# Optimization experiments

Measured on AMD Instinct MI355X. Metric: run time of the kernel, lower is better.

## Reference

```python
import jax, jax.numpy as jnp
import numpy as np

EPS_DIAG = 1e-4
EPS_SOFT = 1e-5
SCALE_DIV = 100000.0


def _cov2cor(x):
    # x: [N, C, d, d]; scale rows and cols by 1/sqrt(|diag|) (== D^-1 @ x @ D^-1)
    dia = jnp.abs(jnp.diagonal(x, axis1=-2, axis2=-1))          # [N, C, d]
    inv = 1.0 / jnp.sqrt(jnp.maximum(dia, EPS_DIAG))
    cor = x * inv[..., :, None] * inv[..., None, :]
    return jnp.clip(cor, -1.0, 1.0)


def _soft_pd_max(x):
    # x: [N, C, d, d]
    x = x - jnp.max(x, axis=(2, 3), keepdims=True)
    e = jnp.exp(x)
    dia = jnp.sum(e, axis=-1)                                    # [N, C, d]
    dia = jnp.maximum(dia, jnp.sum(dia, axis=2, keepdims=True) / SCALE_DIV)
    dia = jnp.maximum(dia, EPS_SOFT)
    inv = 1.0 / jnp.sqrt(dia)
    return e * inv[..., :, None] * inv[..., None, :]


def setup_inputs() -> dict:
    key = jax.random.key(0)
    k0, k1, k2, k3 = jax.random.split(key, 4)
    N, C, d = 64, 64, 64
    inputs = jax.random.normal(k0, (N, C, d, d), dtype=jnp.float32)
    # NonNeg uniform [0, 2/C] init for queries/keys
    w_queries = jax.random.uniform(k1, (C, C), dtype=jnp.float32, minval=0.0, maxval=2.0 / C)
    w_keys = jax.random.uniform(k2, (C, C), dtype=jnp.float32, minval=0.0, maxval=2.0 / C)
    # values: |N(0, 1/sqrt(C))| column-L1-normalized
    wv = jnp.abs(jax.random.normal(k3, (C, C), dtype=jnp.float32) / jnp.sqrt(jnp.float32(C)))
    w_values = wv / jnp.sum(wv, axis=0)
    return {"inputs": inputs, "w_queries": w_queries, "w_keys": w_keys, "w_values": w_values}


def reference(inputs, w_queries, w_keys, w_values):
    cor = _cov2cor(inputs)                                       # [N, C, d, d]
    X = jnp.transpose(cor, (0, 2, 3, 1))                         # [N, d, d, C]
    XWQ = jnp.matmul(X, w_queries)                               # [N, d, d, C]
    XWK = jnp.matmul(X, w_keys)
    XWV = jnp.matmul(X, w_values)
    XWQt = jnp.transpose(XWQ, (0, 3, 1, 2))                      # [N, C, d, d]
    XWKt = jnp.transpose(XWK, (0, 3, 2, 1))                      # [N, C, d, d] (transposed within dxd)
    XWKT = jnp.transpose(XWK, (0, 3, 1, 2))
    A_pre = jnp.matmul(jnp.matmul(XWKt, XWQt), XWKT)             # [N, C, d, d]
    A = _soft_pd_max(A_pre)
    V = jnp.transpose(XWV, (0, 3, 1, 2))                         # [N, C, d, d]
    AXA = jnp.matmul(jnp.matmul(A, V), jnp.transpose(A, (0, 1, 3, 2)))
    return inputs + AXA
```

## Files before the change

kernel.cpp:

```cpp
#include <hip/hip_runtime.h>

#define PITCH 72
#define ZP 136

typedef __attribute__((ext_vector_type(8))) short short8v;
typedef __attribute__((ext_vector_type(4))) short short4v;
typedef __attribute__((ext_vector_type(4))) float f32x4;

__device__ __forceinline__ short f2bf(float v) {
    unsigned u = __builtin_bit_cast(unsigned, v);
    unsigned r = (u + 0x7FFFu + ((u >> 16) & 1u)) >> 16;
    return (short)r;
}
__device__ __forceinline__ float bf2f(short s) {
    unsigned u = ((unsigned)(unsigned short)s) << 16;
    return __builtin_bit_cast(float, u);
}

#define MFMA(a, b, c) __builtin_amdgcn_mfma_f32_16x16x32_bf16(a, b, c, 0, 0, 0)

__device__ __forceinline__ short8v ldfrag(const short* p, int rowtile, int kc, int l) {
    return *(const short8v*)&p[(rowtile * 16 + (l & 15)) * PITCH + kc * 32 + (l >> 4) * 8];
}
__device__ __forceinline__ short8v gfrag(const short* __restrict__ p, int rowtile, int kc, int l) {
    return *(const short8v*)&p[(rowtile * 16 + (l & 15)) * 64 + kc * 32 + (l >> 4) * 8];
}

__device__ __forceinline__ void p1(const short* xh, const short* yh,
                                   int w, int l, f32x4 (&acc)[4]) {
#pragma unroll
    for (int ct = 0; ct < 4; ++ct) acc[ct] = (f32x4){0.f, 0.f, 0.f, 0.f};
#pragma unroll
    for (int kc = 0; kc < 2; ++kc) {
        short8v aH = ldfrag(xh, w, kc, l);
#pragma unroll
        for (int ct = 0; ct < 4; ++ct)
            acc[ct] = MFMA(aH, ldfrag(yh, ct, kc, l), acc[ct]);
    }
}

__device__ __forceinline__ void p1_g(const short* __restrict__ xg, const short* yh,
                                     int w, int l, f32x4 (&acc)[4]) {
#pragma unroll
    for (int ct = 0; ct < 4; ++ct) acc[ct] = (f32x4){0.f, 0.f, 0.f, 0.f};
#pragma unroll
    for (int kc = 0; kc < 2; ++kc) {
        short8v aH = gfrag(xg, w, kc, l);
#pragma unroll
        for (int ct = 0; ct < 4; ++ct)
            acc[ct] = MFMA(aH, ldfrag(yh, ct, kc, l), acc[ct]);
    }
}

__device__ __forceinline__ void p2v_g(const short* __restrict__ xg,
                                      const short* yh, const short* yl,
                                      int w, int l, f32x4 (&acc)[4]) {
#pragma unroll
    for (int ct = 0; ct < 4; ++ct) acc[ct] = (f32x4){0.f, 0.f, 0.f, 0.f};
#pragma unroll
    for (int kc = 0; kc < 2; ++kc) {
        short8v aH = gfrag(xg, w, kc, l);
#pragma unroll
        for (int ct = 0; ct < 4; ++ct) {
            acc[ct] = MFMA(aH, ldfrag(yh, ct, kc, l), acc[ct]);
            acc[ct] = MFMA(aH, ldfrag(yl, ct, kc, l), acc[ct]);
        }
    }
}

__device__ __forceinline__ void p2a(const short* xh, const short* xl,
                                    const short* yh,
                                    int w, int l, f32x4 (&acc)[4]) {
#pragma unroll
    for (int ct = 0; ct < 4; ++ct) acc[ct] = (f32x4){0.f, 0.f, 0.f, 0.f};
#pragma unroll
    for (int kc = 0; kc < 2; ++kc) {
        short8v aH = ldfrag(xh, w, kc, l);
        short8v aL = ldfrag(xl, w, kc, l);
#pragma unroll
        for (int ct = 0; ct < 4; ++ct) {
            short8v bH = ldfrag(yh, ct, kc, l);
            acc[ct] = MFMA(aH, bH, acc[ct]);
            acc[ct] = MFMA(aL, bH, acc[ct]);
        }
    }
}

__device__ __forceinline__ void pack1(const f32x4 (&acc)[4], short* zh, int w, int l) {
    int m0 = w * 16 + (l >> 4) * 4;
#pragma unroll
    for (int ct = 0; ct < 4; ++ct) {
        int n = ct * 16 + (l & 15);
        short4v h;
#pragma unroll
        for (int r = 0; r < 4; ++r) h[r] = f2bf(acc[ct][r]);
        *(short4v*)&zh[n * PITCH + m0] = h;
    }
}

__device__ __forceinline__ void idtrans_ip1(short* pa, int w, int l) {
    short8v a0 = ldfrag(pa, w, 0, l);
    short8v a1 = ldfrag(pa, w, 1, l);
    short8v I0, I1;
#pragma unroll
    for (int j = 0; j < 8; ++j) {
        int bit = 8 * (l >> 4) + j;
        I0[j] = (bit == (l & 15))      ? (short)0x3F80 : (short)0;
        I1[j] = (bit == (l & 15) + 16) ? (short)0x3F80 : (short)0;
    }
    __syncthreads();
    int m0 = w * 16 + (l >> 4) * 4;
    const f32x4 z4 = {0.f, 0.f, 0.f, 0.f};
#pragma unroll
    for (int s = 0; s < 4; ++s) {
        f32x4 d = MFMA((s >> 1) ? a1 : a0, (s & 1) ? I1 : I0, z4);
        short4v ha;
#pragma unroll
        for (int r = 0; r < 4; ++r) ha[r] = f2bf(d[r]);
        *(short4v*)&pa[(s * 16 + (l & 15)) * PITCH + m0] = ha;
    }
}

__device__ __forceinline__ void idtrans_ip2(short* pa, short* pb, int w, int l) {
    short8v a0 = ldfrag(pa, w, 0, l);
    short8v a1 = ldfrag(pa, w, 1, l);
    short8v b0 = ldfrag(pb, w, 0, l);
    short8v b1 = ldfrag(pb, w, 1, l);
    short8v I0, I1;
#pragma unroll
    for (int j = 0; j < 8; ++j) {
        int bit = 8 * (l >> 4) + j;
        I0[j] = (bit == (l & 15))      ? (short)0x3F80 : (short)0;
        I1[j] = (bit == (l & 15) + 16) ? (short)0x3F80 : (short)0;
    }
    __syncthreads();
    int m0 = w * 16 + (l >> 4) * 4;
    const f32x4 z4 = {0.f, 0.f, 0.f, 0.f};
#pragma unroll
    for (int s = 0; s < 4; ++s) {
        f32x4 d = MFMA((s >> 1) ? a1 : a0, (s & 1) ? I1 : I0, z4);
        f32x4 e = MFMA((s >> 1) ? b1 : b0, (s & 1) ? I1 : I0, z4);
        short4v ha, hb2;
#pragma unroll
        for (int r = 0; r < 4; ++r) { ha[r] = f2bf(d[r]); hb2[r] = f2bf(e[r]); }
        int drow = s * 16 + (l & 15);
        *(short4v*)&pa[drow * PITCH + m0] = ha;
        *(short4v*)&pb[drow * PITCH + m0] = hb2;
    }
}

__global__ __launch_bounds__(256) void k0_invdiag(const float* __restrict__ x,
                                                  float* __restrict__ invd) {
    int t = blockIdx.x * 256 + threadIdx.x;
    int nc = t >> 6, k = t & 63;
    float v = fabsf(x[(size_t)nc * 4096 + (size_t)k * 65]);
    invd[t] = rsqrtf(fmaxf(v, 1e-4f));
}

__global__ __launch_bounds__(256) void k0b_w3(const float* __restrict__ wq,
                                              const float* __restrict__ wk,
                                              const float* __restrict__ wv,
                                              short* __restrict__ w3h) {
    int idx = blockIdx.x * 256 + threadIdx.x;
    int co = idx >> 6, c = idx & 63;
    const float* w = (co < 64) ? wq : (co < 128) ? wk : wv;
    w3h[idx] = f2bf(w[c * 64 + (co & 63)]);
}

__global__ __launch_bounds__(256, 3) void k1_mix_mfma(
    const float* __restrict__ x, const float* __restrict__ invd,
    const short* __restrict__ w3h,
    short* __restrict__ Qh, short* __restrict__ Kh, short* __restrict__ Vh)
{
    __shared__ __align__(16) short smem[192 * ZP];
    short* ch0 = smem;
    short* ch1 = smem + 4608;

    const int b = blockIdx.x, n = b >> 5, ip = b & 31;
    const int t = threadIdx.x, l = t & 63, w = t >> 6;
    const size_t nbase = (size_t)n * 64;
    const int i0 = ip * 2;

#pragma unroll
    for (int rep = 0; rep < 8; ++rep) {
        int id = rep * 256 + t;
        int isel = id >> 10, rem = id & 1023;
        int c = rem >> 4, j4 = (rem & 15) * 4;
        int i = i0 + isel;
        float4 xv = *(const float4*)&x[((nbase + c) * 64 + i) * 64 + j4];
        float ii = invd[(nbase + c) * 64 + i];
        float4 jv = *(const float4*)&invd[(nbase + c) * 64 + j4];
        float vv[4] = {xv.x * ii * jv.x, xv.y * ii * jv.y,
                       xv.z * ii * jv.z, xv.w * ii * jv.w};
        short4v h;
#pragma unroll
        for (int r = 0; r < 4; ++r)
            h[r] = f2bf(fminf(1.0f, fmaxf(-1.0f, vv[r])));
        short* dst = isel ? ch1 : ch0;
        *(short4v*)&dst[c * PITCH + j4] = h;
    }
    __syncthreads();
    idtrans_ip2(ch0, ch1, w, l);
    __syncthreads();

    f32x4 a0[4][3], a1[4][3];
#pragma unroll
    for (int jt = 0; jt < 4; ++jt)
#pragma unroll
        for (int cc = 0; cc < 3; ++cc) {
            a0[jt][cc] = (f32x4){0.f, 0.f, 0.f, 0.f};
            a1[jt][cc] = (f32x4){0.f, 0.f, 0.f, 0.f};
        }
#pragma unroll
    for (int kc = 0; kc < 2; ++kc) {
        short8v f0[4], f1[4];
#pragma unroll
        for (int jt = 0; jt < 4; ++jt) {
            f0[jt] = ldfrag(ch0, jt, kc, l);
            f1[jt] = ldfrag(ch1, jt, kc, l);
        }
#pragma unroll
        for (int cc = 0; cc < 3; ++cc) {
            short8v bH = gfrag(w3h, w * 3 + cc, kc, l);
#pragma unroll
            for (int jt = 0; jt < 4; ++jt) {
                a0[jt][cc] = MFMA(f0[jt], bH, a0[jt][cc]);
                a1[jt][cc] = MFMA(f1[jt], bH, a1[jt][cc]);
            }
        }
    }
    __syncthreads();

    {
        int m0 = (l >> 4) * 4, nb = l & 15;
#pragma unroll
        for (int cc = 0; cc < 3; ++cc) {
            int nrow = (w * 3 + cc) * 16 + nb;
#pragma unroll
            for (int jt = 0; jt < 4; ++jt) {
                short4v h0, h1;
#pragma unroll
                for (int r = 0; r < 4; ++r) {
                    h0[r] = f2bf(a0[jt][cc][r]);
                    h1[r] = f2bf(a1[jt][cc][r]);
                }
                *(short4v*)&smem[nrow * ZP + jt * 16 + m0]      = h0;
                *(short4v*)&smem[nrow * ZP + 64 + jt * 16 + m0] = h1;
            }
        }
    }
    __syncthreads();

#pragma unroll
    for (int rep = 0; rep < 12; ++rep) {
        int id = rep * 256 + t;
        int row = id >> 4, c8 = (id & 15) * 8;
        short8v v = *(short8v*)&smem[row * ZP + c8];
        size_t off = (size_t)i0 * 64 + c8;
        if (rep < 4) {
            *(short8v*)&Qh[(nbase + row) * 4096 + off] = v;
        } else if (rep < 8) {
            *(short8v*)&Kh[(nbase + row - 64) * 4096 + off] = v;
        } else {
            *(short8v*)&Vh[(nbase + row - 128) * 4096 + off] = v;
        }
    }
}

__global__ __launch_bounds__(256, 5) void k2_attn_mfma(
    const float* __restrict__ x,
    const short* __restrict__ Qh, const short* __restrict__ Kh,
    const short* __restrict__ Vh,
    float* __restrict__ out)
{
    __shared__ __align__(16) short P[3][4608];
    __shared__ float part[4][64];
    __shared__ float invs[64];
    __shared__ float red[4];

    const int t = threadIdx.x, l = t & 63, w = t >> 6;
    const int nc = blockIdx.x;
    const size_t gbase = (size_t)nc * 4096;

    const short* qh = Qh + gbase;
    const short* kh = Kh + gbase;
    const short* vh = Vh + gbase;

#pragma unroll
    for (int rep = 0; rep < 4; ++rep) {
        int id = rep * 256 + t;
        int r = id >> 4, c4 = (id & 15) * 4;
        *(short4v*)&P[0][r * PITCH + c4] = *(const short4v*)&kh[r * 64 + c4];
    }
    __syncthreads();

    idtrans_ip1(P[0], w, l);
    __syncthreads();

    f32x4 acc[4];

    p1_g(qh, P[0], w, l, acc);
    pack1(acc, P[1], w, l);
    __syncthreads();

    p1(P[1], P[0], w, l, acc);

    float mx = -1e30f;
#pragma unroll
    for (int ct = 0; ct < 4; ++ct)
#pragma unroll
        for (int r = 0; r < 4; ++r) mx = fmaxf(mx, acc[ct][r]);
#pragma unroll
    for (int off = 1; off < 64; off <<= 1) mx = fmaxf(mx, __shfl_xor(mx, off));
    if (l == 0) red[w] = mx;
    __syncthreads();
    mx = fmaxf(fmaxf(red[0], red[1]), fmaxf(red[2], red[3]));

    float e[4][4];
    float cs[4];
#pragma unroll
    for (int ct = 0; ct < 4; ++ct) {
        float s = 0.f;
#pragma unroll
        for (int r = 0; r < 4; ++r) {
            float ev = __expf(acc[ct][r] - mx);
            e[ct][r] = ev;
            s += ev;
        }
        cs[ct] = s;
    }
#pragma unroll
    for (int ct = 0; ct < 4; ++ct) {
        cs[ct] += __shfl_xor(cs[ct], 16);
        cs[ct] += __shfl_xor(cs[ct], 32);
    }
    if (l < 16) {
#pragma unroll
        for (int ct = 0; ct < 4; ++ct) part[w][ct * 16 + l] = cs[ct];
    }
    __syncthreads();
    if (t < 64) {
        float dia = part[0][t] + part[1][t] + part[2][t] + part[3][t];
        float tot = dia;
#pragma unroll
        for (int off = 1; off < 64; off <<= 1) tot += __shfl_xor(tot, off);
        dia = fmaxf(dia, tot / 100000.0f);
        dia = fmaxf(dia, 1e-5f);
        invs[t] = rsqrtf(dia);
    }
    __syncthreads();

    {
        int m0 = w * 16 + (l >> 4) * 4;
        float ir[4] = {invs[m0], invs[m0 + 1], invs[m0 + 2], invs[m0 + 3]};
        int nb = l & 15;
#pragma unroll
        for (int ct = 0; ct < 4; ++ct) {
            float ic = invs[ct * 16 + nb];
            short4v h, lo;
#pragma unroll
            for (int r = 0; r < 4; ++r) {
                float v = e[ct][r] * ir[r] * ic;
                short hb = f2bf(v);
                h[r]  = hb;
                lo[r] = f2bf(v - bf2f(hb));
            }
            *(short4v*)&P[1][(ct * 16 + nb) * PITCH + m0] = h;
            *(short4v*)&P[0][(ct * 16 + nb) * PITCH + m0] = lo;
        }
    }
    __syncthreads();

    p2v_g(vh, P[1], P[0], w, l, acc);
    pack1(acc, P[2], w, l);
    __syncthreads();

    p2a(P[1], P[0], P[2], w, l, acc);
    __syncthreads();

    {
        float* ofs = (float*)&P[0][0];
        int m0 = w * 16 + (l >> 4) * 4;
        int nb = l & 15;
#pragma unroll
        for (int ct = 0; ct < 4; ++ct)
#pragma unroll
            for (int r = 0; r < 4; ++r)
                ofs[(m0 + r) * 68 + ct * 16 + nb] = acc[ct][r];
    }
    __syncthreads();
    {
        const float* ofs = (const float*)&P[0][0];
#pragma unroll
        for (int rep = 0; rep < 4; ++rep) {
            int id = rep * 256 + t;
            int row = id >> 4, c4 = (id & 15) * 4;
            float4 v  = *(const float4*)&ofs[row * 68 + c4];
            float4 xv = *(const float4*)&x[gbase + (size_t)row * 64 + c4];
            *(float4*)&out[gbase + (size_t)row * 64 + c4] =
                make_float4(xv.x + v.x, xv.y + v.y, xv.z + v.z, xv.w + v.w);
        }
    }
}

extern "C" void kernel_launch(void* const* d_in, const int* in_sizes, int n_in,
                              void* d_out, int out_size, void* d_ws, size_t ws_size,
                              hipStream_t stream) {
    const float* x  = (const float*)d_in[0];
    const float* wq = (const float*)d_in[1];
    const float* wk = (const float*)d_in[2];
    const float* wv = (const float*)d_in[3];
    float* out = (float*)d_out;

    char* wsb = (char*)d_ws;
    float* invd = (float*)wsb;
    short* w3h  = (short*)(wsb + (1 << 20));
    short* Qh   = (short*)(wsb + (2 << 20));
    short* Kh   = Qh + 16777216;
    short* Vh   = Kh + 16777216;

    k0_invdiag<<<1024, 256, 0, stream>>>(x, invd);
    k0b_w3<<<48, 256, 0, stream>>>(wq, wk, wv, w3h);
    k1_mix_mfma<<<2048, 256, 0, stream>>>(x, invd, w3h, Qh, Kh, Vh);
    k2_attn_mfma<<<4096, 256, 0, stream>>>(x, Qh, Kh, Vh, out);
}
```

Before: 92.88 us.

## Store Q/K/V in row-interleaved layout and merge prep kernels

Changes the intermediate Q/K/V layout from three separate [N,C,d,d] arrays to one interleaved buffer indexed by (n, i) rows of 192*64 elements, so k1 writes contiguous 1.5K-element chunks per i row with less LDS staging (smaller shared buffer, two half passes). k2 now reads its per-channel Q/K/V with a large stride of 12288 elements. The two small prep kernels are merged into one launch. This trades write coalescing and occupancy in k1 against strided 128-byte row reads in k2.

```diff
diff --git a/kernel.cpp b/kernel.cpp
--- a/kernel.cpp
+++ b/kernel.cpp
@@ -1,7 +1,7 @@
 #include <hip/hip_runtime.h>
 
 #define PITCH 72
-#define ZP 136
+#define QKV_STRIDE 12288
 
 typedef __attribute__((ext_vector_type(8))) short short8v;
 typedef __attribute__((ext_vector_type(4))) short short4v;
@@ -25,6 +25,10 @@
 __device__ __forceinline__ short8v gfrag(const short* __restrict__ p, int rowtile, int kc, int l) {
     return *(const short8v*)&p[(rowtile * 16 + (l & 15)) * 64 + kc * 32 + (l >> 4) * 8];
 }
+__device__ __forceinline__ short8v gfrag_s(const short* __restrict__ p, int rowtile,
+                                           int kc, int l, int stride) {
+    return *(const short8v*)&p[(rowtile * 16 + (l & 15)) * stride + kc * 32 + (l >> 4) * 8];
+}
 
 __device__ __forceinline__ void p1(const short* xh, const short* yh,
                                    int w, int l, f32x4 (&acc)[4]) {
@@ -45,7 +49,7 @@
     for (int ct = 0; ct < 4; ++ct) acc[ct] = (f32x4){0.f, 0.f, 0.f, 0.f};
 #pragma unroll
     for (int kc = 0; kc < 2; ++kc) {
-        short8v aH = gfrag(xg, w, kc, l);
+        short8v aH = gfrag_s(xg, w, kc, l, QKV_STRIDE);
 #pragma unroll
         for (int ct = 0; ct < 4; ++ct)
             acc[ct] = MFMA(aH, ldfrag(yh, ct, kc, l), acc[ct]);
@@ -59,7 +63,7 @@
     for (int ct = 0; ct < 4; ++ct) acc[ct] = (f32x4){0.f, 0.f, 0.f, 0.f};
 #pragma unroll
     for (int kc = 0; kc < 2; ++kc) {
-        short8v aH = gfrag(xg, w, kc, l);
+        short8v aH = gfrag_s(xg, w, kc, l, QKV_STRIDE);
 #pragma unroll
         for (int ct = 0; ct < 4; ++ct) {
             acc[ct] = MFMA(aH, ldfrag(yh, ct, kc, l), acc[ct]);
@@ -149,32 +153,35 @@
     }
 }
 
-__global__ __launch_bounds__(256) void k0_invdiag(const float* __restrict__ x,
-                                                  float* __restrict__ invd) {
-    int t = blockIdx.x * 256 + threadIdx.x;
-    int nc = t >> 6, k = t & 63;
-    float v = fabsf(x[(size_t)nc * 4096 + (size_t)k * 65]);
-    invd[t] = rsqrtf(fmaxf(v, 1e-4f));
-}
-
-__global__ __launch_bounds__(256) void k0b_w3(const float* __restrict__ wq,
-                                              const float* __restrict__ wk,
-                                              const float* __restrict__ wv,
-                                              short* __restrict__ w3h) {
-    int idx = blockIdx.x * 256 + threadIdx.x;
-    int co = idx >> 6, c = idx & 63;
-    const float* w = (co < 64) ? wq : (co < 128) ? wk : wv;
-    w3h[idx] = f2bf(w[c * 64 + (co & 63)]);
+__global__ __launch_bounds__(256) void k0_prep(const float* __restrict__ x,
+                                               const float* __restrict__ wq,
+                                               const float* __restrict__ wk,
+                                               const float* __restrict__ wv,
+                                               float* __restrict__ invd,
+                                               short* __restrict__ w3h) {
+    int b = blockIdx.x;
+    if (b < 1024) {
+        int t = b * 256 + threadIdx.x;
+        int nc = t >> 6, k = t & 63;
+        float v = fabsf(x[(size_t)nc * 4096 + (size_t)k * 65]);
+        invd[t] = rsqrtf(fmaxf(v, 1e-4f));
+    } else {
+        int idx = (b - 1024) * 256 + threadIdx.x;
+        int co = idx >> 6, c = idx & 63;
+        const float* w = (co < 64) ? wq : (co < 128) ? wk : wv;
+        w3h[idx] = f2bf(w[c * 64 + (co & 63)]);
+    }
 }
 
 __global__ __launch_bounds__(256, 3) void k1_mix_mfma(
     const float* __restrict__ x, const float* __restrict__ invd,
     const short* __restrict__ w3h,
-    short* __restrict__ Qh, short* __restrict__ Kh, short* __restrict__ Vh)
+    short* __restrict__ QKV)
 {
-    __shared__ __align__(16) short smem[192 * ZP];
+    __shared__ __align__(16) short smem[13824];
     short* ch0 = smem;
     short* ch1 = smem + 4608;
+    short* z   = smem;
 
     const int b = blockIdx.x, n = b >> 5, ip = b & 31;
     const int t = threadIdx.x, l = t & 63, w = t >> 6;
@@ -231,46 +238,51 @@
     }
     __syncthreads();
 
-    {
-        int m0 = (l >> 4) * 4, nb = l & 15;
-#pragma unroll
-        for (int cc = 0; cc < 3; ++cc) {
-            int nrow = (w * 3 + cc) * 16 + nb;
-#pragma unroll
-            for (int jt = 0; jt < 4; ++jt) {
-                short4v h0, h1;
-#pragma unroll
-                for (int r = 0; r < 4; ++r) {
-                    h0[r] = f2bf(a0[jt][cc][r]);
-                    h1[r] = f2bf(a1[jt][cc][r]);
-                }
-                *(short4v*)&smem[nrow * ZP + jt * 16 + m0]      = h0;
-                *(short4v*)&smem[nrow * ZP + 64 + jt * 16 + m0] = h1;
-            }
-        }
-    }
-    __syncthreads();
-
-#pragma unroll
-    for (int rep = 0; rep < 12; ++rep) {
+    const int m0 = (l >> 4) * 4, nb = l & 15;
+    short* dst0 = QKV + (size_t)(nbase + i0) * QKV_STRIDE;
+
+#pragma unroll
+    for (int cc = 0; cc < 3; ++cc) {
+        int nrow = (w * 3 + cc) * 16 + nb;
+#pragma unroll
+        for (int jt = 0; jt < 4; ++jt) {
+            short4v h;
+#pragma unroll
+            for (int r = 0; r < 4; ++r) h[r] = f2bf(a0[jt][cc][r]);
+            *(short4v*)&z[nrow * PITCH + jt * 16 + m0] = h;
+        }
+    }
+    __syncthreads();
+#pragma unroll
+    for (int rep = 0; rep < 6; ++rep) {
         int id = rep * 256 + t;
-        int row = id >> 4, c8 = (id & 15) * 8;
-        short8v v = *(short8v*)&smem[row * ZP + c8];
-        size_t off = (size_t)i0 * 64 + c8;
-        if (rep < 4) {
-            *(short8v*)&Qh[(nbase + row) * 4096 + off] = v;
-        } else if (rep < 8) {
-            *(short8v*)&Kh[(nbase + row - 64) * 4096 + off] = v;
-        } else {
-            *(short8v*)&Vh[(nbase + row - 128) * 4096 + off] = v;
-        }
+        *(short8v*)&dst0[id * 8] = *(short8v*)&z[(id >> 3) * PITCH + (id & 7) * 8];
+    }
+    __syncthreads();
+
+#pragma unroll
+    for (int cc = 0; cc < 3; ++cc) {
+        int nrow = (w * 3 + cc) * 16 + nb;
+#pragma unroll
+        for (int jt = 0; jt < 4; ++jt) {
+            short4v h;
+#pragma unroll
+            for (int r = 0; r < 4; ++r) h[r] = f2bf(a1[jt][cc][r]);
+            *(short4v*)&z[nrow * PITCH + jt * 16 + m0] = h;
+        }
+    }
+    __syncthreads();
+#pragma unroll
+    for (int rep = 0; rep < 6; ++rep) {
+        int id = rep * 256 + t;
+        *(short8v*)&dst0[QKV_STRIDE + id * 8] =
+            *(short8v*)&z[(id >> 3) * PITCH + (id & 7) * 8];
     }
 }
 
 __global__ __launch_bounds__(256, 5) void k2_attn_mfma(
     const float* __restrict__ x,
-    const short* __restrict__ Qh, const short* __restrict__ Kh,
-    const short* __restrict__ Vh,
+    const short* __restrict__ QKV,
     float* __restrict__ out)
 {
     __shared__ __align__(16) short P[3][4608];
@@ -279,18 +291,19 @@
     __shared__ float red[4];
 
     const int t = threadIdx.x, l = t & 63, w = t >> 6;
-    const int nc = blockIdx.x;
+    const int nc = blockIdx.x, n = nc >> 6, c = nc & 63;
     const size_t gbase = (size_t)nc * 4096;
 
-    const short* qh = Qh + gbase;
-    const short* kh = Kh + gbase;
-    const short* vh = Vh + gbase;
+    const short* qh = QKV + (size_t)n * 64 * QKV_STRIDE + (size_t)c * 64;
+    const short* kh = qh + 64 * 64;
+    const short* vh = qh + 128 * 64;
 
 #pragma unroll
     for (int rep = 0; rep < 4; ++rep) {
         int id = rep * 256 + t;
         int r = id >> 4, c4 = (id & 15) * 4;
-        *(short4v*)&P[0][r * PITCH + c4] = *(const short4v*)&kh[r * 64 + c4];
+        *(short4v*)&P[0][r * PITCH + c4] =
+            *(const short4v*)&kh[r * QKV_STRIDE + c4];
     }
     __syncthreads();
 
@@ -415,12 +428,9 @@
     char* wsb = (char*)d_ws;
     float* invd = (float*)wsb;
     short* w3h  = (short*)(wsb + (1 << 20));
-    short* Qh   = (short*)(wsb + (2 << 20));
-    short* Kh   = Qh + 16777216;
-    short* Vh   = Kh + 16777216;
-
-    k0_invdiag<<<1024, 256, 0, stream>>>(x, invd);
-    k0b_w3<<<48, 256, 0, stream>>>(wq, wk, wv, w3h);
-    k1_mix_mfma<<<2048, 256, 0, stream>>>(x, invd, w3h, Qh, Kh, Vh);
-    k2_attn_mfma<<<4096, 256, 0, stream>>>(x, Qh, Kh, Vh, out);
-}
+    short* QKV  = (short*)(wsb + (2 << 20));
+
+    k0_prep<<<1072, 256, 0, stream>>>(x, wq, wk, wv, invd, w3h);
+    k1_mix_mfma<<<2048, 256, 0, stream>>>(x, invd, w3h, QKV);
+    k2_attn_mfma<<<4096, 256, 0, stream>>>(x, QKV, out);
+}
```

New measurement: 80.63 us. 13.2% less time.
